# Kernel tuning notes

Measured on AMD Instinct MI355X. Metric: run time of the kernel, lower is better.

The kernel has to match this reference:

```python
import jax, jax.numpy as jnp
import numpy as np

B, T, C = 4, 2048, 1024
N_HEADS = 16
HEAD_DIM = C // N_HEADS


def setup_inputs() -> dict:
    key = jax.random.key(0)
    k1, k2, k3 = jax.random.split(key, 3)
    x = jax.random.normal(k1, (B, T, C), dtype=jnp.float32)
    w_qkv = jax.random.normal(k2, (C, 3 * C), dtype=jnp.float32) * (1.0 / np.sqrt(C))
    w_proj = jax.random.normal(k3, (C, C), dtype=jnp.float32) * (1.0 / np.sqrt(C))
    return {"x": x, "w_qkv": w_qkv, "w_proj": w_proj}


def reference(x, w_qkv, w_proj):
    b, t, c = x.shape
    qkv = x @ w_qkv                                  # [B,T,3C]
    q, k, v = jnp.split(qkv, 3, axis=-1)
    def split_heads(u):
        return u.reshape(b, t, N_HEADS, HEAD_DIM).transpose(0, 2, 1, 3)  # [B,H,T,D]
    q, k, v = split_heads(q), split_heads(k), split_heads(v)
    scale = 1.0 / np.sqrt(HEAD_DIM)
    att = jnp.einsum('bhqd,bhkd->bhqk', q, k) * scale   # [B,H,T,T]
    causal = jnp.tril(jnp.ones((t, t), dtype=bool))
    att = jnp.where(causal[None, None], att, -jnp.inf)
    att = jax.nn.softmax(att, axis=-1)
    out = jnp.einsum('bhqk,bhkd->bhqd', att, v)         # [B,H,T,D]
    out = out.transpose(0, 2, 1, 3).reshape(b, t, c)
    return out @ w_proj
```

## Files before the change

kernel.cpp:

```cpp
#include <hip/hip_runtime.h>
#include <hip/hip_bf16.h>
#include <stdint.h>

typedef __bf16 bf16_t;
typedef __bf16 bf16x4 __attribute__((ext_vector_type(4)));
typedef __bf16 bf16x8 __attribute__((ext_vector_type(8)));
typedef float  f32x4  __attribute__((ext_vector_type(4)));

#define B_    4
#define T_    2048
#define C_    1024
#define NH    16
#define HD    64
#define M_TOT (B_ * T_)

__device__ __forceinline__ void gload16(const void* g, void* l) {
    __builtin_amdgcn_global_load_lds(
        (const __attribute__((address_space(1))) uint32_t*)g,
        (__attribute__((address_space(3))) uint32_t*)l, 16, 0, 0);
}

__global__ void conv_x_kernel(const float* __restrict__ x, bf16_t* __restrict__ xb, int n4) {
    int i = blockIdx.x * blockDim.x + threadIdx.x;
    int stride = gridDim.x * blockDim.x;
    for (; i < n4; i += stride) {
        float4 v = reinterpret_cast<const float4*>(x)[i];
        union { bf16_t h[4]; uint2 u; } p;
        p.h[0] = (bf16_t)v.x; p.h[1] = (bf16_t)v.y;
        p.h[2] = (bf16_t)v.z; p.h[3] = (bf16_t)v.w;
        reinterpret_cast<uint2*>(xb)[i] = p.u;
    }
}

__global__ void transpose_w_kernel(const float* __restrict__ w, bf16_t* __restrict__ wt,
                                   int K, int N) {
    __shared__ float tile[32][33];
    int n0 = blockIdx.x * 32, k0 = blockIdx.y * 32;
    int tx = threadIdx.x, ty = threadIdx.y;
    #pragma unroll
    for (int i = 0; i < 32; i += 8)
        tile[ty + i][tx] = w[(size_t)(k0 + ty + i) * N + n0 + tx];
    __syncthreads();
    #pragma unroll
    for (int i = 0; i < 32; i += 8)
        wt[(size_t)(n0 + ty + i) * K + k0 + tx] = (bf16_t)tile[tx][ty + i];
}

#define QSCALE 0.18033688011112042f

#define LA0 0
#define LA1 16384
#define LB0 32768
#define LB1 49152

#define GST(ptr, rbase, base, kt) do { int k0_ = ((kt) << 6) & (K - 1);           \
    _Pragma("unroll") for (int c_ = 0; c_ < 4; ++c_) {                            \
        int li_ = tid + c_ * 256; int row_ = li_ >> 3;                            \
        int sw_ = (li_ & 7) ^ (row_ & 7);                                         \
        gload16(ptr + (size_t)((rbase) + row_) * K + k0_ + sw_ * 8,               \
                lds + (base) + li_ * 16); } } while (0)

#define GREAD(abase, bbase) do {                                                  \
    _Pragma("unroll") for (int mi_ = 0; mi_ < 4; ++mi_)                           \
        _Pragma("unroll") for (int kk_ = 0; kk_ < 2; ++kk_) {                     \
            int row_  = wm * 64 + mi_ * 16 + q16;                                 \
            int byte_ = (row_ * 128 + kk_ * 64 + g * 16) ^ ((row_ & 7) << 4);     \
            af[mi_ * 2 + kk_] = *reinterpret_cast<const bf16x8*>(lds + (abase) + byte_); } \
    _Pragma("unroll") for (int n_ = 0; n_ < 4; ++n_)                              \
        _Pragma("unroll") for (int kk_ = 0; kk_ < 2; ++kk_) {                     \
            int row_  = wn * 64 + n_ * 16 + q16;                                  \
            int byte_ = (row_ * 128 + kk_ * 64 + g * 16) ^ ((row_ & 7) << 4);     \
            bfr[n_ * 2 + kk_] = *reinterpret_cast<const bf16x8*>(lds + (bbase) + byte_); } } while (0)

#define GMFMA(milo) do { __builtin_amdgcn_s_setprio(1);                           \
    _Pragma("unroll") for (int mi_ = 0; mi_ < 2; ++mi_)                           \
        _Pragma("unroll") for (int kk_ = 0; kk_ < 2; ++kk_)                       \
            _Pragma("unroll") for (int n_ = 0; n_ < 4; ++n_)                      \
                acc[(milo) + mi_][n_] = __builtin_amdgcn_mfma_f32_16x16x32_bf16(  \
                    af[((milo) + mi_) * 2 + kk_], bfr[n_ * 2 + kk_],              \
                    acc[(milo) + mi_][n_], 0, 0, 0);                              \
    __builtin_amdgcn_s_setprio(0); } while (0)

template<int MODE>
__global__ __launch_bounds__(256, 2) void gemm_kernel(
    const bf16_t* __restrict__ A, const bf16_t* __restrict__ Bt,
    float* __restrict__ Cout,
    bf16_t* __restrict__ Qo, bf16_t* __restrict__ Ko, bf16_t* __restrict__ Vt,
    int M, int N, int K)
{
    __shared__ __align__(16) char lds[65536];
    const int tid  = threadIdx.x;
    const int lane = tid & 63;
    const int wid  = tid >> 6;
    const int wm   = wid >> 1, wn = wid & 1;
    const int q16  = lane & 15, g = lane >> 4;
    const int xcd = blockIdx.x & 7;
    const int i0  = blockIdx.x >> 3;
    const int mbase = (xcd * 8 + (i0 & 7)) * 128;
    const int nbase = (i0 >> 3) * 128;
    const int NITER = K >> 7;

    f32x4  acc[4][4] = {};
    bf16x8 af[8], bfr[8];

    GST(A, mbase, LA0, 0); GST(Bt, nbase, LB0, 0);
    GST(A, mbase, LA1, 1); GST(Bt, nbase, LB1, 1);
    asm volatile("s_waitcnt vmcnt(8)" ::: "memory");
    __builtin_amdgcn_s_barrier();
    __builtin_amdgcn_sched_barrier(0);

    #pragma unroll 1
    for (int i = 0; i < NITER; ++i) {
        GREAD(LA0, LB0);
        __builtin_amdgcn_s_barrier();
        asm volatile("s_waitcnt lgkmcnt(0)" ::: "memory");
        __builtin_amdgcn_sched_barrier(0);
        GMFMA(0);
        __builtin_amdgcn_s_barrier();
        GST(A, mbase, LA0, 2 * i + 2); GST(Bt, nbase, LB0, 2 * i + 2);
        __builtin_amdgcn_sched_barrier(0);
        GMFMA(2);
        asm volatile("s_waitcnt vmcnt(8)" ::: "memory");
        __builtin_amdgcn_s_barrier();
        GREAD(LA1, LB1);
        __builtin_amdgcn_s_barrier();
        asm volatile("s_waitcnt lgkmcnt(0)" ::: "memory");
        __builtin_amdgcn_sched_barrier(0);
        GMFMA(0);
        __builtin_amdgcn_s_barrier();
        GST(A, mbase, LA1, 2 * i + 3); GST(Bt, nbase, LB1, 2 * i + 3);
        __builtin_amdgcn_sched_barrier(0);
        GMFMA(2);
        asm volatile("s_waitcnt vmcnt(8)" ::: "memory");
        __builtin_amdgcn_s_barrier();
    }
    asm volatile("s_waitcnt vmcnt(0)" ::: "memory");

    #pragma unroll
    for (int mi = 0; mi < 4; ++mi) {
        #pragma unroll
        for (int n = 0; n < 4; ++n) {
            const int row0 = mbase + wm * 64 + mi * 16 + g * 4;
            const int col0 = nbase + wn * 64 + n * 16;
            if (MODE == 0) {
                #pragma unroll
                for (int r = 0; r < 4; ++r)
                    Cout[(size_t)(row0 + r) * N + col0 + q16] = acc[mi][n][r];
            } else {
                const int b = row0 >> 11, t0 = row0 & 2047;
                if (col0 < 1024) {
                    int h = col0 >> 6, d = (col0 & 63) + q16;
                    #pragma unroll
                    for (int r = 0; r < 4; ++r)
                        Qo[((size_t)(b * NH + h) * T_ + t0 + r) * HD + d] =
                            (bf16_t)(acc[mi][n][r] * QSCALE);
                } else if (col0 < 2048) {
                    int h = (col0 - 1024) >> 6, d = (col0 & 63) + q16;
                    #pragma unroll
                    for (int r = 0; r < 4; ++r)
                        Ko[((size_t)(b * NH + h) * T_ + t0 + r) * HD + d] =
                            (bf16_t)acc[mi][n][r];
                } else {
                    int h = (col0 - 2048) >> 6, d = (col0 & 63) + q16;
                    bf16x4 vv = { (bf16_t)acc[mi][n][0], (bf16_t)acc[mi][n][1],
                                  (bf16_t)acc[mi][n][2], (bf16_t)acc[mi][n][3] };
                    *reinterpret_cast<bf16x4*>(
                        Vt + ((size_t)(b * NH + h) * HD + d) * T_ + t0) = vv;
                }
            }
        }
    }
}

__global__ __launch_bounds__(256, 3) void attn_kernel(
    const bf16_t* __restrict__ Q, const bf16_t* __restrict__ K,
    const bf16_t* __restrict__ Vt, bf16_t* __restrict__ out)
{
    __shared__ __align__(16) char kvbuf[2][16384];
    __shared__ __align__(16) char plds[4][4096];
    const int tid  = threadIdx.x;
    const int lane = tid & 63;
    const int wid  = tid >> 6;
    const int g    = lane >> 4;
    const int q16  = lane & 15;

    const int bid = blockIdx.x;
    const int k   = bid >> 6;
    const int bh  = bid & 63;
    const int b   = bh >> 4, h = bh & 15;
    const int qt  = (k < 4) ? (15 - k) : (k < 8) ? (k + 4) : (k < 12) ? (k - 4) : (15 - k);

    const bf16_t* Qh = Q  + (size_t)bh * T_ * HD;
    const bf16_t* Kh = K  + (size_t)bh * T_ * HD;
    const bf16_t* Vh = Vt + (size_t)bh * HD * T_;
    char* myp = plds[wid];
    const int pswz = (q16 & 7) << 4;

#define STAGE(buf, kv0) do {                                                     \
        _Pragma("unroll") for (int c = 0; c < 2; ++c) {                          \
            int li  = tid + c * 256;                                             \
            int row = li >> 3;                                                   \
            int sw  = (li & 7) ^ (row & 7);                                      \
            gload16(Kh + (size_t)((kv0) + row) * HD + sw * 8, (char*)(buf) + li * 16);          \
            gload16(Vh + (size_t)row * T_ + (kv0) + sw * 8, (char*)(buf) + 8192 + li * 16);     \
        } } while (0)

    const int nt    = 2 * qt + 2;
    const int qbase = qt * 128 + wid * 32;
    const int qg0   = qbase + q16;
    const int qg1   = qbase + 16 + q16;

    bf16x8 qf0[2], qf1[2];
    #pragma unroll
    for (int kk = 0; kk < 2; ++kk) {
        qf0[kk] = *reinterpret_cast<const bf16x8*>(Qh + (size_t)qg0 * HD + kk * 32 + g * 8);
        qf1[kk] = *reinterpret_cast<const bf16x8*>(Qh + (size_t)qg1 * HD + kk * 32 + g * 8);
    }

    f32x4 acc0[4] = {}, acc1[4] = {};
    float l0 = 0.f, l1 = 0.f;

    STAGE(kvbuf[0], 0);
    int cur = 0;
    for (int it = 0; it < nt; ++it) {
        const int kv0 = it << 6;
        if (it + 1 < nt) {
            STAGE(kvbuf[cur ^ 1], (it + 1) << 6);
            asm volatile("s_waitcnt vmcnt(4)" ::: "memory");
        } else {
            asm volatile("s_waitcnt vmcnt(0)" ::: "memory");
        }
        __builtin_amdgcn_s_barrier();
        __builtin_amdgcn_sched_barrier(0);
        const char* Kl = kvbuf[cur];
        const char* Vl = kvbuf[cur] + 8192;

        f32x4 s0[4] = {}, s1[4] = {};
        __builtin_amdgcn_s_setprio(1);
        #pragma unroll
        for (int t = 0; t < 4; ++t) {
            #pragma unroll
            for (int kk = 0; kk < 2; ++kk) {
                int row  = t * 16 + q16;
                int byte = (row * 128 + kk * 64 + g * 16) ^ ((row & 7) << 4);
                bf16x8 kf = *reinterpret_cast<const bf16x8*>(Kl + byte);
                s0[t] = __builtin_amdgcn_mfma_f32_16x16x32_bf16(kf, qf0[kk], s0[t], 0, 0, 0);
                s1[t] = __builtin_amdgcn_mfma_f32_16x16x32_bf16(kf, qf1[kk], s1[t], 0, 0, 0);
            }
        }
        __builtin_amdgcn_s_setprio(0);
        if (kv0 + 63 > qbase) {
            #pragma unroll
            for (int t = 0; t < 4; ++t)
                #pragma unroll
                for (int r = 0; r < 4; ++r) {
                    int kv = kv0 + t * 16 + g * 4 + r;
                    if (kv > qg0) s0[t][r] = -1e30f;
                    if (kv > qg1) s1[t][r] = -1e30f;
                }
        }
        #pragma unroll
        for (int t = 0; t < 4; ++t) {
            float p00 = exp2f(s0[t][0]), p01 = exp2f(s0[t][1]);
            float p02 = exp2f(s0[t][2]), p03 = exp2f(s0[t][3]);
            l0 += (p00 + p01) + (p02 + p03);
            bf16x4 pw0 = { (bf16_t)p00, (bf16_t)p01, (bf16_t)p02, (bf16_t)p03 };
            int byte = (q16 * 128 + t * 32 + g * 8) ^ pswz;
            *reinterpret_cast<bf16x4*>(myp + byte) = pw0;
            float p10 = exp2f(s1[t][0]), p11 = exp2f(s1[t][1]);
            float p12 = exp2f(s1[t][2]), p13 = exp2f(s1[t][3]);
            l1 += (p10 + p11) + (p12 + p13);
            bf16x4 pw1 = { (bf16_t)p10, (bf16_t)p11, (bf16_t)p12, (bf16_t)p13 };
            *reinterpret_cast<bf16x4*>(myp + 2048 + byte) = pw1;
        }
        asm volatile("s_waitcnt lgkmcnt(0)" ::: "memory");
        __builtin_amdgcn_sched_barrier(0);
        bf16x8 pf0[2], pf1[2];
        #pragma unroll
        for (int kk2 = 0; kk2 < 2; ++kk2) {
            int byte = (q16 * 128 + kk2 * 64 + g * 16) ^ pswz;
            pf0[kk2] = *reinterpret_cast<const bf16x8*>(myp + byte);
            pf1[kk2] = *reinterpret_cast<const bf16x8*>(myp + 2048 + byte);
        }
        __builtin_amdgcn_s_setprio(1);
        #pragma unroll
        for (int nf = 0; nf < 4; ++nf) {
            #pragma unroll
            for (int kk2 = 0; kk2 < 2; ++kk2) {
                int row  = nf * 16 + q16;
                int byte = (row * 128 + kk2 * 64 + g * 16) ^ ((row & 7) << 4);
                bf16x8 vf = *reinterpret_cast<const bf16x8*>(Vl + byte);
                acc0[nf] = __builtin_amdgcn_mfma_f32_16x16x32_bf16(vf, pf0[kk2], acc0[nf], 0, 0, 0);
                acc1[nf] = __builtin_amdgcn_mfma_f32_16x16x32_bf16(vf, pf1[kk2], acc1[nf], 0, 0, 0);
            }
        }
        __builtin_amdgcn_s_setprio(0);
        __syncthreads();
        cur ^= 1;
    }
    l0 += __shfl_xor(l0, 16, 64);
    l0 += __shfl_xor(l0, 32, 64);
    l1 += __shfl_xor(l1, 16, 64);
    l1 += __shfl_xor(l1, 32, 64);
    float inv0 = 1.f / l0, inv1 = 1.f / l1;
    #pragma unroll
    for (int nf = 0; nf < 4; ++nf) {
        bf16x4 ov0 = { (bf16_t)(acc0[nf][0] * inv0), (bf16_t)(acc0[nf][1] * inv0),
                       (bf16_t)(acc0[nf][2] * inv0), (bf16_t)(acc0[nf][3] * inv0) };
        *reinterpret_cast<bf16x4*>(
            out + (size_t)(b * T_ + qg0) * C_ + h * HD + nf * 16 + g * 4) = ov0;
        bf16x4 ov1 = { (bf16_t)(acc1[nf][0] * inv1), (bf16_t)(acc1[nf][1] * inv1),
                       (bf16_t)(acc1[nf][2] * inv1), (bf16_t)(acc1[nf][3] * inv1) };
        *reinterpret_cast<bf16x4*>(
            out + (size_t)(b * T_ + qg1) * C_ + h * HD + nf * 16 + g * 4) = ov1;
    }
#undef STAGE
}

extern "C" void kernel_launch(void* const* d_in, const int* in_sizes, int n_in,
                              void* d_out, int out_size, void* d_ws, size_t ws_size,
                              hipStream_t stream) {
    const float* x      = (const float*)d_in[0];
    const float* w_qkv  = (const float*)d_in[1];
    const float* w_proj = (const float*)d_in[2];
    float* out = (float*)d_out;

    char* ws = (char*)d_ws;
    bf16_t* xb     = (bf16_t*)(ws);
    bf16_t* wqkvT  = (bf16_t*)(ws + 16777216);
    bf16_t* wprojT = (bf16_t*)(ws + 23068672);
    bf16_t* Qb     = (bf16_t*)(ws + 25165824);
    bf16_t* Kb     = (bf16_t*)(ws + 41943040);
    bf16_t* Vtb    = (bf16_t*)(ws + 58720256);
    bf16_t* attnb  = (bf16_t*)(ws + 75497472);

    conv_x_kernel<<<2048, 256, 0, stream>>>(x, xb, (B_ * T_ * C_) / 4);
    transpose_w_kernel<<<dim3(3 * C_ / 32, C_ / 32), dim3(32, 8), 0, stream>>>(w_qkv, wqkvT, C_, 3 * C_);
    transpose_w_kernel<<<dim3(C_ / 32, C_ / 32), dim3(32, 8), 0, stream>>>(w_proj, wprojT, C_, C_);

    gemm_kernel<1><<<1536, 256, 0, stream>>>(
        xb, wqkvT, nullptr, Qb, Kb, Vtb, M_TOT, 3 * C_, C_);

    attn_kernel<<<1024, 256, 0, stream>>>(Qb, Kb, Vtb, attnb);

    gemm_kernel<0><<<512, 256, 0, stream>>>(
        attnb, wprojT, out, nullptr, nullptr, nullptr, M_TOT, C_, C_);
}
```

Measured before the change: 164.2 us.

## Enlarge attention query tile to 256 rows per block, 64 per wave

The attention kernel now processes 256 query rows per block (64 per wave, four 16-row sub-tiles) instead of 128, halving the grid to 512 blocks. Each K/V tile loaded into LDS is reused across twice as many queries, which cuts staging traffic and barriers per unit of work. Waves whose queries lie entirely before a KV tile now skip its compute. The cost is more registers (occupancy bound drops from 3 to 2), a larger P buffer in LDS, coarser load balancing across fewer blocks, and more wasted causal tiles per block.

```diff
diff --git a/kernel.cpp b/kernel.cpp
--- a/kernel.cpp
+++ b/kernel.cpp
@@ -172,12 +172,12 @@
     }
 }
 
-__global__ __launch_bounds__(256, 3) void attn_kernel(
+__global__ __launch_bounds__(256, 2) void attn_kernel(
     const bf16_t* __restrict__ Q, const bf16_t* __restrict__ K,
     const bf16_t* __restrict__ Vt, bf16_t* __restrict__ out)
 {
     __shared__ __align__(16) char kvbuf[2][16384];
-    __shared__ __align__(16) char plds[4][4096];
+    __shared__ __align__(16) char plds[4][8192];
     const int tid  = threadIdx.x;
     const int lane = tid & 63;
     const int wid  = tid >> 6;
@@ -188,7 +188,7 @@
     const int k   = bid >> 6;
     const int bh  = bid & 63;
     const int b   = bh >> 4, h = bh & 15;
-    const int qt  = (k < 4) ? (15 - k) : (k < 8) ? (k + 4) : (k < 12) ? (k - 4) : (15 - k);
+    const int qt  = (k < 4) ? (7 - k) : (k - 4);
 
     const bf16_t* Qh = Q  + (size_t)bh * T_ * HD;
     const bf16_t* Kh = K  + (size_t)bh * T_ * HD;
@@ -205,20 +205,19 @@
             gload16(Vh + (size_t)row * T_ + (kv0) + sw * 8, (char*)(buf) + 8192 + li * 16);     \
         } } while (0)
 
-    const int nt    = 2 * qt + 2;
-    const int qbase = qt * 128 + wid * 32;
-    const int qg0   = qbase + q16;
-    const int qg1   = qbase + 16 + q16;
-
-    bf16x8 qf0[2], qf1[2];
-    #pragma unroll
-    for (int kk = 0; kk < 2; ++kk) {
-        qf0[kk] = *reinterpret_cast<const bf16x8*>(Qh + (size_t)qg0 * HD + kk * 32 + g * 8);
-        qf1[kk] = *reinterpret_cast<const bf16x8*>(Qh + (size_t)qg1 * HD + kk * 32 + g * 8);
-    }
-
-    f32x4 acc0[4] = {}, acc1[4] = {};
-    float l0 = 0.f, l1 = 0.f;
+    const int nt    = 4 * (qt + 1);
+    const int qbase = qt * 256 + wid * 64;
+
+    bf16x8 qf[4][2];
+    #pragma unroll
+    for (int s = 0; s < 4; ++s)
+        #pragma unroll
+        for (int kk = 0; kk < 2; ++kk)
+            qf[s][kk] = *reinterpret_cast<const bf16x8*>(
+                Qh + (size_t)(qbase + s * 16 + q16) * HD + kk * 32 + g * 8);
+
+    f32x4 acc[4][4] = {};
+    float lsum[4] = {0.f, 0.f, 0.f, 0.f};
 
     STAGE(kvbuf[0], 0);
     int cur = 0;
@@ -232,87 +231,97 @@
         }
         __builtin_amdgcn_s_barrier();
         __builtin_amdgcn_sched_barrier(0);
-        const char* Kl = kvbuf[cur];
-        const char* Vl = kvbuf[cur] + 8192;
-
-        f32x4 s0[4] = {}, s1[4] = {};
-        __builtin_amdgcn_s_setprio(1);
-        #pragma unroll
-        for (int t = 0; t < 4; ++t) {
+
+        if (kv0 <= qbase + 63) {
+            const char* Kl = kvbuf[cur];
+            const char* Vl = kvbuf[cur] + 8192;
+
+            bf16x8 kf[8];
             #pragma unroll
-            for (int kk = 0; kk < 2; ++kk) {
-                int row  = t * 16 + q16;
-                int byte = (row * 128 + kk * 64 + g * 16) ^ ((row & 7) << 4);
-                bf16x8 kf = *reinterpret_cast<const bf16x8*>(Kl + byte);
-                s0[t] = __builtin_amdgcn_mfma_f32_16x16x32_bf16(kf, qf0[kk], s0[t], 0, 0, 0);
-                s1[t] = __builtin_amdgcn_mfma_f32_16x16x32_bf16(kf, qf1[kk], s1[t], 0, 0, 0);
+            for (int t = 0; t < 4; ++t)
+                #pragma unroll
+                for (int kk = 0; kk < 2; ++kk) {
+                    int row  = t * 16 + q16;
+                    int byte = (row * 128 + kk * 64 + g * 16) ^ ((row & 7) << 4);
+                    kf[t * 2 + kk] = *reinterpret_cast<const bf16x8*>(Kl + byte);
+                }
+            const bool diag = (kv0 + 63 > qbase);
+            #pragma unroll
+            for (int s = 0; s < 4; ++s) {
+                f32x4 s4[4] = {};
+                __builtin_amdgcn_s_setprio(1);
+                #pragma unroll
+                for (int t = 0; t < 4; ++t)
+                    #pragma unroll
+                    for (int kk = 0; kk < 2; ++kk)
+                        s4[t] = __builtin_amdgcn_mfma_f32_16x16x32_bf16(
+                            kf[t * 2 + kk], qf[s][kk], s4[t], 0, 0, 0);
+                __builtin_amdgcn_s_setprio(0);
+                if (diag) {
+                    const int qg = qbase + s * 16 + q16;
+                    #pragma unroll
+                    for (int t = 0; t < 4; ++t)
+                        #pragma unroll
+                        for (int r = 0; r < 4; ++r)
+                            if (kv0 + t * 16 + g * 4 + r > qg) s4[t][r] = -1e30f;
+                }
+                #pragma unroll
+                for (int t = 0; t < 4; ++t) {
+                    float p0 = exp2f(s4[t][0]), p1 = exp2f(s4[t][1]);
+                    float p2 = exp2f(s4[t][2]), p3 = exp2f(s4[t][3]);
+                    lsum[s] += (p0 + p1) + (p2 + p3);
+                    bf16x4 pw = { (bf16_t)p0, (bf16_t)p1, (bf16_t)p2, (bf16_t)p3 };
+                    int byte = (q16 * 128 + t * 32 + g * 8) ^ pswz;
+                    *reinterpret_cast<bf16x4*>(myp + s * 2048 + byte) = pw;
+                }
+            }
+            asm volatile("s_waitcnt lgkmcnt(0)" ::: "memory");
+            __builtin_amdgcn_sched_barrier(0);
+
+            bf16x8 vf[8];
+            #pragma unroll
+            for (int nf = 0; nf < 4; ++nf)
+                #pragma unroll
+                for (int kk2 = 0; kk2 < 2; ++kk2) {
+                    int row  = nf * 16 + q16;
+                    int byte = (row * 128 + kk2 * 64 + g * 16) ^ ((row & 7) << 4);
+                    vf[nf * 2 + kk2] = *reinterpret_cast<const bf16x8*>(Vl + byte);
+                }
+            #pragma unroll
+            for (int s = 0; s < 4; ++s) {
+                bf16x8 pf[2];
+                #pragma unroll
+                for (int kk2 = 0; kk2 < 2; ++kk2) {
+                    int byte = (q16 * 128 + kk2 * 64 + g * 16) ^ pswz;
+                    pf[kk2] = *reinterpret_cast<const bf16x8*>(myp + s * 2048 + byte);
+                }
+                __builtin_amdgcn_s_setprio(1);
+                #pragma unroll
+                for (int nf = 0; nf < 4; ++nf)
+                    #pragma unroll
+                    for (int kk2 = 0; kk2 < 2; ++kk2)
+                        acc[s][nf] = __builtin_amdgcn_mfma_f32_16x16x32_bf16(
+                            vf[nf * 2 + kk2], pf[kk2], acc[s][nf], 0, 0, 0);
+                __builtin_amdgcn_s_setprio(0);
             }
         }
-        __builtin_amdgcn_s_setprio(0);
-        if (kv0 + 63 > qbase) {
-            #pragma unroll
-            for (int t = 0; t < 4; ++t)
-                #pragma unroll
-                for (int r = 0; r < 4; ++r) {
-                    int kv = kv0 + t * 16 + g * 4 + r;
-                    if (kv > qg0) s0[t][r] = -1e30f;
-                    if (kv > qg1) s1[t][r] = -1e30f;
-                }
-        }
-        #pragma unroll
-        for (int t = 0; t < 4; ++t) {
-            float p00 = exp2f(s0[t][0]), p01 = exp2f(s0[t][1]);
-            float p02 = exp2f(s0[t][2]), p03 = exp2f(s0[t][3]);
-            l0 += (p00 + p01) + (p02 + p03);
-            bf16x4 pw0 = { (bf16_t)p00, (bf16_t)p01, (bf16_t)p02, (bf16_t)p03 };
-            int byte = (q16 * 128 + t * 32 + g * 8) ^ pswz;
-            *reinterpret_cast<bf16x4*>(myp + byte) = pw0;
-            float p10 = exp2f(s1[t][0]), p11 = exp2f(s1[t][1]);
-            float p12 = exp2f(s1[t][2]), p13 = exp2f(s1[t][3]);
-            l1 += (p10 + p11) + (p12 + p13);
-            bf16x4 pw1 = { (bf16_t)p10, (bf16_t)p11, (bf16_t)p12, (bf16_t)p13 };
-            *reinterpret_cast<bf16x4*>(myp + 2048 + byte) = pw1;
-        }
-        asm volatile("s_waitcnt lgkmcnt(0)" ::: "memory");
-        __builtin_amdgcn_sched_barrier(0);
-        bf16x8 pf0[2], pf1[2];
-        #pragma unroll
-        for (int kk2 = 0; kk2 < 2; ++kk2) {
-            int byte = (q16 * 128 + kk2 * 64 + g * 16) ^ pswz;
-            pf0[kk2] = *reinterpret_cast<const bf16x8*>(myp + byte);
-            pf1[kk2] = *reinterpret_cast<const bf16x8*>(myp + 2048 + byte);
-        }
-        __builtin_amdgcn_s_setprio(1);
+        __syncthreads();
+        cur ^= 1;
+    }
+    #pragma unroll
+    for (int s = 0; s < 4; ++s) {
+        float l = lsum[s];
+        l += __shfl_xor(l, 16, 64);
+        l += __shfl_xor(l, 32, 64);
+        float inv = 1.f / l;
+        const int qg = qbase + s * 16 + q16;
         #pragma unroll
         for (int nf = 0; nf < 4; ++nf) {
-            #pragma unroll
-            for (int kk2 = 0; kk2 < 2; ++kk2) {
-                int row  = nf * 16 + q16;
-                int byte = (row * 128 + kk2 * 64 + g * 16) ^ ((row & 7) << 4);
-                bf16x8 vf = *reinterpret_cast<const bf16x8*>(Vl + byte);
-                acc0[nf] = __builtin_amdgcn_mfma_f32_16x16x32_bf16(vf, pf0[kk2], acc0[nf], 0, 0, 0);
-                acc1[nf] = __builtin_amdgcn_mfma_f32_16x16x32_bf16(vf, pf1[kk2], acc1[nf], 0, 0, 0);
-            }
+            bf16x4 ov = { (bf16_t)(acc[s][nf][0] * inv), (bf16_t)(acc[s][nf][1] * inv),
+                          (bf16_t)(acc[s][nf][2] * inv), (bf16_t)(acc[s][nf][3] * inv) };
+            *reinterpret_cast<bf16x4*>(
+                out + (size_t)(b * T_ + qg) * C_ + h * HD + nf * 16 + g * 4) = ov;
         }
-        __builtin_amdgcn_s_setprio(0);
-        __syncthreads();
-        cur ^= 1;
-    }
-    l0 += __shfl_xor(l0, 16, 64);
-    l0 += __shfl_xor(l0, 32, 64);
-    l1 += __shfl_xor(l1, 16, 64);
-    l1 += __shfl_xor(l1, 32, 64);
-    float inv0 = 1.f / l0, inv1 = 1.f / l1;
-    #pragma unroll
-    for (int nf = 0; nf < 4; ++nf) {
-        bf16x4 ov0 = { (bf16_t)(acc0[nf][0] * inv0), (bf16_t)(acc0[nf][1] * inv0),
-                       (bf16_t)(acc0[nf][2] * inv0), (bf16_t)(acc0[nf][3] * inv0) };
-        *reinterpret_cast<bf16x4*>(
-            out + (size_t)(b * T_ + qg0) * C_ + h * HD + nf * 16 + g * 4) = ov0;
-        bf16x4 ov1 = { (bf16_t)(acc1[nf][0] * inv1), (bf16_t)(acc1[nf][1] * inv1),
-                       (bf16_t)(acc1[nf][2] * inv1), (bf16_t)(acc1[nf][3] * inv1) };
-        *reinterpret_cast<bf16x4*>(
-            out + (size_t)(b * T_ + qg1) * C_ + h * HD + nf * 16 + g * 4) = ov1;
     }
 #undef STAGE
 }
@@ -341,7 +350,7 @@
     gemm_kernel<1><<<1536, 256, 0, stream>>>(
         xb, wqkvT, nullptr, Qb, Kb, Vtb, M_TOT, 3 * C_, C_);
 
-    attn_kernel<<<1024, 256, 0, stream>>>(Qb, Kb, Vtb, attnb);
+    attn_kernel<<<512, 256, 0, stream>>>(Qb, Kb, Vtb, attnb);
 
     gemm_kernel<0><<<512, 256, 0, stream>>>(
         attnb, wprojT, out, nullptr, nullptr, nullptr, M_TOT, C_, C_);
```

Result: slower. 181.4 us (+10.5%).
